# Performance work log

Measured on AMD Instinct MI355X. Metric: run time of the kernel, lower is better.

The kernel has to match this reference:

```python
import jax, jax.numpy as jnp
import numpy as np

BATCH, SEQ, IN, HID, CLS = 512, 1024, 64, 256, 10

def setup_inputs() -> dict:
    key = jax.random.key(0)
    k1, k2, k3, k4, k5 = jax.random.split(key, 5)
    s_ih = 1.0 / np.sqrt(IN + HID)
    s_ho = 1.0 / np.sqrt(HID)
    return {
        "inputs": jax.random.normal(k1, (BATCH, SEQ, IN), dtype=jnp.float32),
        "W_ih": jax.random.normal(k2, (IN + HID, HID), dtype=jnp.float32) * s_ih,
        "b_ih": jax.random.normal(k3, (HID,), dtype=jnp.float32) * s_ih,
        "W_ho": jax.random.normal(k4, (HID, CLS), dtype=jnp.float32) * s_ho,
        "b_ho": jax.random.normal(k5, (CLS,), dtype=jnp.float32) * s_ho,
    }

def reference(inputs, W_ih, b_ih, W_ho, b_ho):
    # Elman RNN: hidden_{t} = tanh([x_t, hidden_{t-1}] @ W_ih + b_ih)
    B, S, I = inputs.shape
    H = W_ih.shape[1]
    # split W_ih into input and hidden blocks (equivalent to concat+matmul)
    Wx = W_ih[:I]      # (I, H)
    Wh = W_ih[I:]      # (H, H)
    h0 = jnp.zeros((B, H), dtype=inputs.dtype)
    # precompute input projections for all timesteps at once: (B, S, H)
    xproj = jnp.einsum('bsi,ih->bsh', inputs, Wx) + b_ih

    def step(h, xp_t):
        h_new = jnp.tanh(xp_t + h @ Wh)
        return h_new, None

    h_final, _ = jax.lax.scan(step, h0, jnp.swapaxes(xproj, 0, 1))  # scan over time
    return h_final @ W_ho + b_ho  # (B, CLS)
```

## Files before the change

kernel.cpp:

```cpp
#include <hip/hip_runtime.h>
#include <hip/hip_bf16.h>


#define BATCH 512
#define SEQ   1024
#define INP   64
#define HID   256
#define CLS   10
#define NTHREADS 512
#define TSCALE 2.8853900817779268f

typedef short bf16x8 __attribute__((ext_vector_type(8)));
typedef float f32x4  __attribute__((ext_vector_type(4)));

static __device__ __forceinline__ unsigned short f2bf(float f) {
  __hip_bfloat16 h = __float2bfloat16(f);
  return *reinterpret_cast<unsigned short*>(&h);
}
static __device__ __forceinline__ float bf2f(unsigned short b) {
  union { unsigned int u; float f; } v; v.u = ((unsigned int)b) << 16;
  return v.f;
}
static __device__ __forceinline__ unsigned int cvt_pk_bf16(float lo, float hi) {
  unsigned int r;
  asm("v_cvt_pk_bf16_f32 %0, %1, %2" : "=v"(r) : "v"(lo), "v"(hi));
  return r;
}
static __device__ __forceinline__ float fast_exp2(float x) {
#if __has_builtin(__builtin_amdgcn_exp2f)
  return __builtin_amdgcn_exp2f(x);
#else
  return __exp2f(x);
#endif
}
static __device__ __forceinline__ float fast_rcp(float x) {
#if __has_builtin(__builtin_amdgcn_rcpf)
  return __builtin_amdgcn_rcpf(x);
#else
  return 1.0f / x;
#endif
}
static __device__ __forceinline__ float tanh_scaled(float s) {
  return 1.0f - 2.0f * fast_rcp(1.0f + fast_exp2(s));
}

#define MFMA16(A, B, C) __builtin_amdgcn_mfma_f32_16x16x32_bf16(A, B, C, 0, 0, 0)

#define BARRIER() asm volatile("s_waitcnt lgkmcnt(0)\n\ts_barrier" ::: "memory")

#define STEP(T, CUR, XR) do {                                                   \
        \
    if (wave == 0) {                                                            \
      ((unsigned int*)sX[(CUR) ^ 1])[(xcp >> 4) * 32 + xrow * 16 + (xcp & 15)]  \
          = cvt_pk_bf16(XR.x, XR.y);                                            \
      int tn_ = (T) + 3; tn_ = tn_ < SEQ ? tn_ : SEQ - 1;                       \
      XR = *(const float2*)&xstage[(size_t)tn_ * INP];                          \
    }                                                                           \
    f32x4 acc0a = {bias0, bias0, bias0, bias0};                                 \
    f32x4 acc1a = {bias1, bias1, bias1, bias1};                                 \
    f32x4 acc0b = {0.f, 0.f, 0.f, 0.f};                                         \
    f32x4 acc1b = {0.f, 0.f, 0.f, 0.f};                                         \
                         \
    if (frow < 2) {                                                             \
      aP0 = *(const bf16x8*)&sX[CUR][0][frow][g8];                              \
      aP1 = *(const bf16x8*)&sX[CUR][1][frow][g8];                              \
      aQ0 = *(const bf16x8*)&sH[CUR][0][frow][g8];                              \
      aQ1 = *(const bf16x8*)&sH[CUR][1][frow][g8];                              \
    }                                                                           \
    __builtin_amdgcn_s_setprio(1);                                              \
    acc0a = MFMA16(aP0, bw[0][0], acc0a); acc1a = MFMA16(aP0, bw[0][1], acc1a); \
    acc0b = MFMA16(aP1, bw[1][0], acc0b); acc1b = MFMA16(aP1, bw[1][1], acc1b); \
    __builtin_amdgcn_sched_barrier(0);                                          \
    if (frow < 2) {                                                             \
      aP0 = *(const bf16x8*)&sH[CUR][2][frow][g8];                              \
      aP1 = *(const bf16x8*)&sH[CUR][3][frow][g8];                              \
    }                                                                           \
    acc0a = MFMA16(aQ0, bw[2][0], acc0a); acc1a = MFMA16(aQ0, bw[2][1], acc1a); \
    acc0b = MFMA16(aQ1, bw[3][0], acc0b); acc1b = MFMA16(aQ1, bw[3][1], acc1b); \
    __builtin_amdgcn_sched_barrier(0);                                          \
    if (frow < 2) {                                                             \
      aQ0 = *(const bf16x8*)&sH[CUR][4][frow][g8];                              \
      aQ1 = *(const bf16x8*)&sH[CUR][5][frow][g8];                              \
    }                                                                           \
    acc0a = MFMA16(aP0, bw[4][0], acc0a); acc1a = MFMA16(aP0, bw[4][1], acc1a); \
    acc0b = MFMA16(aP1, bw[5][0], acc0b); acc1b = MFMA16(aP1, bw[5][1], acc1b); \
    __builtin_amdgcn_sched_barrier(0);                                          \
    if (frow < 2) {                                                             \
      aP0 = *(const bf16x8*)&sH[CUR][6][frow][g8];                              \
      aP1 = *(const bf16x8*)&sH[CUR][7][frow][g8];                              \
    }                                                                           \
    acc0a = MFMA16(aQ0, bw[6][0], acc0a); acc1a = MFMA16(aQ0, bw[6][1], acc1a); \
    acc0b = MFMA16(aQ1, bw[7][0], acc0b); acc1b = MFMA16(aQ1, bw[7][1], acc1b); \
    __builtin_amdgcn_sched_barrier(0);                                          \
    acc0a = MFMA16(aP0, bw[8][0], acc0a); acc1a = MFMA16(aP0, bw[8][1], acc1a); \
    acc0b = MFMA16(aP1, bw[9][0], acc0b); acc1b = MFMA16(aP1, bw[9][1], acc1b); \
    __builtin_amdgcn_s_setprio(0);                                              \
            \
    float t00 = tanh_scaled(acc0a[0] + acc0b[0]);       \
    float t10 = tanh_scaled(acc1a[0] + acc1b[0]);       \
    float t01 = tanh_scaled(acc0a[1] + acc0b[1]);       \
    float t11 = tanh_scaled(acc1a[1] + acc1b[1]);       \
    if (g == 0) {                                                               \
      unsigned int* hd_ = (unsigned int*)sH[(CUR) ^ 1];                         \
      hd_[wave * 32 + frow]      = cvt_pk_bf16(t00, t10);            \
      hd_[wave * 32 + 16 + frow] = cvt_pk_bf16(t01, t11);            \
    }                                                                           \
    BARRIER();                                                                  \
  } while (0)

__global__ __launch_bounds__(NTHREADS, 2)
void rnn_scan_kernel(const float* __restrict__ x,
                     const float* __restrict__ W_ih,
                     const float* __restrict__ b_ih,
                     const float* __restrict__ W_ho,
                     const float* __restrict__ b_ho,
                     float* __restrict__ out) {
  __shared__ __align__(16) unsigned short sH[2][8][2][32];
  __shared__ __align__(16) unsigned short sX[2][2][2][32];

  const int tid  = threadIdx.x;
  const int lane = tid & 63;
  const int wave = tid >> 6;
  const int b0   = blockIdx.x * 2;

  const int g    = (lane >> 4) & 3;
  const int g8   = g * 8;
  const int frow = lane & 15;

  bf16x8 bw[10][2];
  const int colE = 32 * wave + 2 * frow;
  const float bias0 = b_ih[colE] * TSCALE;
  const float bias1 = b_ih[colE + 1] * TSCALE;
#pragma unroll
  for (int q = 0; q < 2; ++q) {
#pragma unroll
    for (int kt = 0; kt < 10; ++kt) {
      bf16x8 v;
#pragma unroll
      for (int i = 0; i < 8; ++i)
        v[i] = (short)f2bf(W_ih[(size_t)(kt * 32 + g * 8 + i) * HID + colE + q] * TSCALE);
      bw[kt][q] = v;
    }
  }

  const int xrow = lane >> 5, xcp = lane & 31;
  const float* xstage = x + (size_t)(b0 + xrow) * SEQ * INP + xcp * 2;
  float2 xrA = make_float2(0.f, 0.f), xrB = make_float2(0.f, 0.f);

  bf16x8 aP0 = {}, aP1 = {}, aQ0 = {}, aQ1 = {};

  if (tid < 256) ((unsigned int*)sH[0])[tid] = 0u;
  if (wave == 0) {
    float2 v0 = *(const float2*)&xstage[0];
    ((unsigned int*)sX[0])[(xcp >> 4) * 32 + xrow * 16 + (xcp & 15)]
        = cvt_pk_bf16(v0.x, v0.y);
    xrA = *(const float2*)&xstage[(size_t)1 * INP];
    xrB = *(const float2*)&xstage[(size_t)2 * INP];
  }
  BARRIER();

#pragma unroll 1
  for (int t = 0; t < SEQ; t += 2) {
    STEP(t,     0, xrA);
    STEP(t + 1, 1, xrB);
  }

  if (tid < 2 * CLS) {
    const int r = tid / CLS, cl = tid - r * CLS;
    float s = b_ho[cl];
#pragma unroll 8
    for (int k = 0; k < HID; ++k)
      s += bf2f(sH[0][k >> 5][r][k & 31]) * W_ho[(size_t)k * CLS + cl];
    out[(size_t)(b0 + r) * CLS + cl] = s;
  }
}

extern "C" void kernel_launch(void* const* d_in, const int* in_sizes, int n_in,
                              void* d_out, int out_size, void* d_ws, size_t ws_size,
                              hipStream_t stream) {
  const float* x    = (const float*)d_in[0];
  const float* W_ih = (const float*)d_in[1];
  const float* b_ih = (const float*)d_in[2];
  const float* W_ho = (const float*)d_in[3];
  const float* b_ho = (const float*)d_in[4];
  float* out = (float*)d_out;

  rnn_scan_kernel<<<BATCH / 2, NTHREADS, 0, stream>>>(x, W_ih, b_ih, W_ho, b_ho, out);
}
```

Before: 529.3 us.

## Spread x staging across all waves and drop MFMA scheduling barriers

Input staging for the next timestep now uses 8 lanes in each of the 8 waves instead of all of wave 0, balancing global-load latency across waves. The MFMA chain is restructured to use six register fragments with fewer, earlier LDS loads. The sched_barrier and setprio hints are removed so the compiler can interleave freely. The unused accumulator rows are no longer seeded with bias. The risk is that without the scheduling barriers the compiler may serialize LDS waits before the MFMAs.

```diff
diff --git a/kernel.cpp b/kernel.cpp
--- a/kernel.cpp
+++ b/kernel.cpp
@@ -49,52 +49,45 @@
 #define BARRIER() asm volatile("s_waitcnt lgkmcnt(0)\n\ts_barrier" ::: "memory")
 
 #define STEP(T, CUR, XR) do {                                                   \
-        \
-    if (wave == 0) {                                                            \
-      ((unsigned int*)sX[(CUR) ^ 1])[(xcp >> 4) * 32 + xrow * 16 + (xcp & 15)]  \
+     \
+     \
+    if (lane < 8) {                                                             \
+      ((unsigned int*)sX[(CUR) ^ 1])[((scp >> 4) * 2 + srow) * 16 + (scp & 15)] \
           = cvt_pk_bf16(XR.x, XR.y);                                            \
       int tn_ = (T) + 3; tn_ = tn_ < SEQ ? tn_ : SEQ - 1;                       \
       XR = *(const float2*)&xstage[(size_t)tn_ * INP];                          \
     }                                                                           \
-    f32x4 acc0a = {bias0, bias0, bias0, bias0};                                 \
-    f32x4 acc1a = {bias1, bias1, bias1, bias1};                                 \
+    f32x4 acc0a = {bias0, bias0, 0.f, 0.f};                                     \
+    f32x4 acc1a = {bias1, bias1, 0.f, 0.f};                                     \
     f32x4 acc0b = {0.f, 0.f, 0.f, 0.f};                                         \
     f32x4 acc1b = {0.f, 0.f, 0.f, 0.f};                                         \
-                         \
+        \
     if (frow < 2) {                                                             \
-      aP0 = *(const bf16x8*)&sX[CUR][0][frow][g8];                              \
-      aP1 = *(const bf16x8*)&sX[CUR][1][frow][g8];                              \
-      aQ0 = *(const bf16x8*)&sH[CUR][0][frow][g8];                              \
-      aQ1 = *(const bf16x8*)&sH[CUR][1][frow][g8];                              \
+      fA = *(const bf16x8*)&sX[CUR][0][frow][g8];                               \
+      fB = *(const bf16x8*)&sX[CUR][1][frow][g8];                               \
+      fC = *(const bf16x8*)&sH[CUR][0][frow][g8];                               \
+      fD = *(const bf16x8*)&sH[CUR][1][frow][g8];                               \
+      fE = *(const bf16x8*)&sH[CUR][2][frow][g8];                               \
+      fF = *(const bf16x8*)&sH[CUR][3][frow][g8];                               \
     }                                                                           \
-    __builtin_amdgcn_s_setprio(1);                                              \
-    acc0a = MFMA16(aP0, bw[0][0], acc0a); acc1a = MFMA16(aP0, bw[0][1], acc1a); \
-    acc0b = MFMA16(aP1, bw[1][0], acc0b); acc1b = MFMA16(aP1, bw[1][1], acc1b); \
-    __builtin_amdgcn_sched_barrier(0);                                          \
+    acc0a = MFMA16(fA, bw[0][0], acc0a); acc1a = MFMA16(fA, bw[0][1], acc1a);   \
+    acc0b = MFMA16(fB, bw[1][0], acc0b); acc1b = MFMA16(fB, bw[1][1], acc1b);   \
     if (frow < 2) {                                                             \
-      aP0 = *(const bf16x8*)&sH[CUR][2][frow][g8];                              \
-      aP1 = *(const bf16x8*)&sH[CUR][3][frow][g8];                              \
+      fA = *(const bf16x8*)&sH[CUR][4][frow][g8];                               \
+      fB = *(const bf16x8*)&sH[CUR][5][frow][g8];                               \
     }                                                                           \
-    acc0a = MFMA16(aQ0, bw[2][0], acc0a); acc1a = MFMA16(aQ0, bw[2][1], acc1a); \
-    acc0b = MFMA16(aQ1, bw[3][0], acc0b); acc1b = MFMA16(aQ1, bw[3][1], acc1b); \
-    __builtin_amdgcn_sched_barrier(0);                                          \
+    acc0a = MFMA16(fC, bw[2][0], acc0a); acc1a = MFMA16(fC, bw[2][1], acc1a);   \
+    acc0b = MFMA16(fD, bw[3][0], acc0b); acc1b = MFMA16(fD, bw[3][1], acc1b);   \
     if (frow < 2) {                                                             \
-      aQ0 = *(const bf16x8*)&sH[CUR][4][frow][g8];                              \
-      aQ1 = *(const bf16x8*)&sH[CUR][5][frow][g8];                              \
+      fC = *(const bf16x8*)&sH[CUR][6][frow][g8];                               \
+      fD = *(const bf16x8*)&sH[CUR][7][frow][g8];                               \
     }                                                                           \
-    acc0a = MFMA16(aP0, bw[4][0], acc0a); acc1a = MFMA16(aP0, bw[4][1], acc1a); \
-    acc0b = MFMA16(aP1, bw[5][0], acc0b); acc1b = MFMA16(aP1, bw[5][1], acc1b); \
-    __builtin_amdgcn_sched_barrier(0);                                          \
-    if (frow < 2) {                                                             \
-      aP0 = *(const bf16x8*)&sH[CUR][6][frow][g8];                              \
-      aP1 = *(const bf16x8*)&sH[CUR][7][frow][g8];                              \
-    }                                                                           \
-    acc0a = MFMA16(aQ0, bw[6][0], acc0a); acc1a = MFMA16(aQ0, bw[6][1], acc1a); \
-    acc0b = MFMA16(aQ1, bw[7][0], acc0b); acc1b = MFMA16(aQ1, bw[7][1], acc1b); \
-    __builtin_amdgcn_sched_barrier(0);                                          \
-    acc0a = MFMA16(aP0, bw[8][0], acc0a); acc1a = MFMA16(aP0, bw[8][1], acc1a); \
-    acc0b = MFMA16(aP1, bw[9][0], acc0b); acc1b = MFMA16(aP1, bw[9][1], acc1b); \
-    __builtin_amdgcn_s_setprio(0);                                              \
+    acc0a = MFMA16(fE, bw[4][0], acc0a); acc1a = MFMA16(fE, bw[4][1], acc1a);   \
+    acc0b = MFMA16(fF, bw[5][0], acc0b); acc1b = MFMA16(fF, bw[5][1], acc1b);   \
+    acc0a = MFMA16(fA, bw[6][0], acc0a); acc1a = MFMA16(fA, bw[6][1], acc1a);   \
+    acc0b = MFMA16(fB, bw[7][0], acc0b); acc1b = MFMA16(fB, bw[7][1], acc1b);   \
+    acc0a = MFMA16(fC, bw[8][0], acc0a); acc1a = MFMA16(fC, bw[8][1], acc1a);   \
+    acc0b = MFMA16(fD, bw[9][0], acc0b); acc1b = MFMA16(fD, bw[9][1], acc1b);   \
             \
     float t00 = tanh_scaled(acc0a[0] + acc0b[0]);       \
     float t10 = tanh_scaled(acc1a[0] + acc1b[0]);       \
@@ -143,16 +136,17 @@
     }
   }
 
-  const int xrow = lane >> 5, xcp = lane & 31;
-  const float* xstage = x + (size_t)(b0 + xrow) * SEQ * INP + xcp * 2;
+  const int slot = wave * 8 + (lane & 7);
+  const int srow = slot >> 5, scp = slot & 31;
+  const float* xstage = x + (size_t)(b0 + srow) * SEQ * INP + scp * 2;
   float2 xrA = make_float2(0.f, 0.f), xrB = make_float2(0.f, 0.f);
 
-  bf16x8 aP0 = {}, aP1 = {}, aQ0 = {}, aQ1 = {};
+  bf16x8 fA = {}, fB = {}, fC = {}, fD = {}, fE = {}, fF = {};
 
   if (tid < 256) ((unsigned int*)sH[0])[tid] = 0u;
-  if (wave == 0) {
+  if (lane < 8) {
     float2 v0 = *(const float2*)&xstage[0];
-    ((unsigned int*)sX[0])[(xcp >> 4) * 32 + xrow * 16 + (xcp & 15)]
+    ((unsigned int*)sX[0])[((scp >> 4) * 2 + srow) * 16 + (scp & 15)]
         = cvt_pk_bf16(v0.x, v0.y);
     xrA = *(const float2*)&xstage[(size_t)1 * INP];
     xrB = *(const float2*)&xstage[(size_t)2 * INP];
```

Result: no change. 537.7 us (+1.6%).
